# Kernel optimization log

Hardware: AMD Instinct MI355X
Metric: run time of the kernel (lower is better)

The kernel has to match this reference:

```python
import jax, jax.numpy as jnp
import numpy as np

K = 1  # Op(k=1): num = num_op // k == num_op, so random.sample selects ALL ops (deterministic)


def setup_inputs() -> dict:
    key = jax.random.key(0)
    k1, k2, k3, k4, k5 = jax.random.split(key, 5)
    N, D = 50000, 128
    NUM_OP, E = 8, 400000
    return {
        "x": jax.random.normal(k1, (N, D), dtype=jnp.float32),
        "edge_vals": jax.random.uniform(k2, (NUM_OP, E), dtype=jnp.float32),
        "ws": jax.random.uniform(k3, (NUM_OP,), dtype=jnp.float32),
        "edge_rows": jax.random.randint(k4, (NUM_OP, E), 0, N, dtype=jnp.int32),
        "edge_cols": jax.random.randint(k5, (NUM_OP, E), 0, N, dtype=jnp.int32),
    }


def reference(x, edge_vals, ws, edge_rows, edge_cols):
    # out = (1/num) * sum_i ws[i] * spmm(A_i, x), with num = num_op (k=1 -> all ops sampled)
    N = x.shape[0]
    num_op = ws.shape[0]
    num = num_op // K
    out = jnp.zeros_like(x)
    for i in range(num_op):  # small fixed set of ops (NAS mixture), not a data dim
        msg = edge_vals[i][:, None] * x[edge_cols[i]]  # [E, D] gather + scale
        out = out + ws[i] * jax.ops.segment_sum(msg, edge_rows[i], num_segments=N)
    return out / num
```

## Files before the change

### kernel.cpp

```cpp
#include <hip/hip_runtime.h>


#define D_DIM 128
#define RPB_SHIFT 5
#define RPB 32
#define CSEG 16
#define CSEG_SHIFT 12
#define NB (RPB * CSEG)
#define MAXB 2048
#define CHUNK 8192
#define SCAN_BLOCK 1024
#define CVT_BLOCKS 1024
#define CNT_BLOCKS 256

typedef unsigned long long ull;

static __device__ __forceinline__ unsigned short f2bf(float f) {
    unsigned int u = __float_as_uint(f);
    u += 0x7FFFu + ((u >> 16) & 1u);
    return (unsigned short)(u >> 16);
}

static __device__ __forceinline__ ull pack2f(float a, float b) {
    return (ull)__float_as_uint(a) | ((ull)__float_as_uint(b) << 32);
}

__global__ __launch_bounds__(256) void spmm_scatter_kernel(
    const float* __restrict__ x, const float* __restrict__ edge_vals,
    const float* __restrict__ ws, const int* __restrict__ edge_rows,
    const int* __restrict__ edge_cols, float* __restrict__ out,
    int E, float inv_num)
{
    const int  op   = blockIdx.y;
    const long base = (long)op * (long)E;
    const float wscale = ws[op] * inv_num;
    const int lane = threadIdx.x & 63;
    const int wave = blockIdx.x * (blockDim.x >> 6) + (threadIdx.x >> 6);
    const int nwaves = gridDim.x * (blockDim.x >> 6);
    for (int e = wave; e < E; e += nwaves) {
        const int row = edge_rows[base + e];
        const int col = edge_cols[base + e];
        const float v = edge_vals[base + e] * wscale;
        const float2 xv = *reinterpret_cast<const float2*>(x + (long)col * D_DIM + lane * 2);
        float* o = out + (long)row * D_DIM + lane * 2;
        atomicAdd(o, xv.x * v);
        atomicAdd(o + 1, xv.y * v);
    }
}

__global__ __launch_bounds__(256) void convert_count_kernel(
    const float4* __restrict__ x4, ull* __restrict__ xh, int n4,
    const int* __restrict__ rows, int* __restrict__ gcount, long n, int B)
{
    __shared__ int h[MAXB];
    if (blockIdx.x < CVT_BLOCKS) {
        const int stride = CVT_BLOCKS * 256;
        for (int i = blockIdx.x * 256 + threadIdx.x; i < n4; i += stride) {
            const float4 v = x4[i];
            const ull p =
                (ull)f2bf(v.x)
                | ((ull)f2bf(v.y) << 16)
                | ((ull)f2bf(v.z) << 32)
                | ((ull)f2bf(v.w) << 48);
            xh[i] = p;
        }
    } else {
        const int cb = blockIdx.x - CVT_BLOCKS;
        for (int i = threadIdx.x; i < B; i += 256) h[i] = 0;
        __syncthreads();
        const long n4r = n >> 2;
        for (long q = (long)cb * 256 + threadIdx.x; q < n4r;
             q += (long)CNT_BLOCKS * 256) {
            const int4 r = reinterpret_cast<const int4*>(rows)[q];
            atomicAdd(&h[r.x >> RPB_SHIFT], 1);
            atomicAdd(&h[r.y >> RPB_SHIFT], 1);
            atomicAdd(&h[r.z >> RPB_SHIFT], 1);
            atomicAdd(&h[r.w >> RPB_SHIFT], 1);
        }
        if (cb == 0 && (long)threadIdx.x < (n & 3))
            atomicAdd(&h[rows[(n4r << 2) + threadIdx.x] >> RPB_SHIFT], 1);
        __syncthreads();
        for (int i = threadIdx.x; i < B; i += 256)
            if (h[i]) atomicAdd(&gcount[i], h[i]);
    }
}

__global__ __launch_bounds__(SCAN_BLOCK) void scan_kernel(
    int* __restrict__ cursors, int* __restrict__ offsets, int N)
{
    __shared__ int sdata[SCAN_BLOCK];
    __shared__ int carry_s;
    if (threadIdx.x == 0) carry_s = 0;
    __syncthreads();
    for (int base = 0; base < N; base += SCAN_BLOCK) {
        const int i = base + (int)threadIdx.x;
        const int v = (i < N) ? cursors[i] : 0;
        sdata[threadIdx.x] = v;
        __syncthreads();
        for (int ofs = 1; ofs < SCAN_BLOCK; ofs <<= 1) {
            int t = (threadIdx.x >= (unsigned)ofs) ? sdata[threadIdx.x - ofs] : 0;
            __syncthreads();
            sdata[threadIdx.x] += t;
            __syncthreads();
        }
        const int incl  = sdata[threadIdx.x];
        const int carry = carry_s;
        if (i < N) {
            const int excl = carry + incl - v;
            offsets[i] = excl;
            cursors[i] = excl;
        }
        __syncthreads();
        if (threadIdx.x == SCAN_BLOCK - 1) carry_s = carry + incl;
        __syncthreads();
    }
    if (threadIdx.x == 0) offsets[N] = carry_s;
}

__global__ __launch_bounds__(1024, 8) void scatter_bucket_kernel(
    const int* __restrict__ edge_rows, const int* __restrict__ edge_cols,
    const float* __restrict__ edge_vals, const float* __restrict__ ws,
    int* __restrict__ gcursor, ull* __restrict__ records,
    int E, float inv_num, int B)
{
    __shared__ int hist[MAXB];
    const int  op   = blockIdx.y;
    const long base = (long)op * (long)E;
    const int  e0   = blockIdx.x * CHUNK;
    const int  e1   = min(e0 + CHUNK, E);
    const float wscale = ws[op] * inv_num;
    const int  tid  = (int)threadIdx.x;
    const int*   erow = edge_rows + base;
    const int*   ecol = edge_cols + base;
    const float* eval = edge_vals + base;

    for (int i = tid; i < B; i += 1024) hist[i] = 0;
    __syncthreads();

    const int gA = e0 + tid * 4;
    const int gB = gA + 4096;
    int4 rA = make_int4(0, 0, 0, 0), rB = make_int4(0, 0, 0, 0);
    int  mA = 0, mB = 0;

    { const int rem = e1 - gA;
      if (rem >= 4) { rA = *reinterpret_cast<const int4*>(erow + gA); mA = 4; }
      else if (rem > 0) { mA = rem; rA.x = erow[gA];
          if (rem > 1) rA.y = erow[gA + 1];
          if (rem > 2) rA.z = erow[gA + 2]; } }
    { const int rem = e1 - gB;
      if (rem >= 4) { rB = *reinterpret_cast<const int4*>(erow + gB); mB = 4; }
      else if (rem > 0) { mB = rem; rB.x = erow[gB];
          if (rem > 1) rB.y = erow[gB + 1];
          if (rem > 2) rB.z = erow[gB + 2]; } }

    if (mA > 0) atomicAdd(&hist[rA.x >> RPB_SHIFT], 1);
    if (mA > 1) atomicAdd(&hist[rA.y >> RPB_SHIFT], 1);
    if (mA > 2) atomicAdd(&hist[rA.z >> RPB_SHIFT], 1);
    if (mA > 3) atomicAdd(&hist[rA.w >> RPB_SHIFT], 1);
    if (mB > 0) atomicAdd(&hist[rB.x >> RPB_SHIFT], 1);
    if (mB > 1) atomicAdd(&hist[rB.y >> RPB_SHIFT], 1);
    if (mB > 2) atomicAdd(&hist[rB.z >> RPB_SHIFT], 1);
    if (mB > 3) atomicAdd(&hist[rB.w >> RPB_SHIFT], 1);
    __syncthreads();

    for (int i = tid; i < B; i += 1024) {
        const int c = hist[i];
        hist[i] = c ? atomicAdd(&gcursor[i], c) : 0;
    }
    __syncthreads();

#define EMIT(RW, CW, VW)                                                       \
    { const int bin_ = (RW) >> RPB_SHIFT;                                      \
      const int pos_ = atomicAdd(&hist[bin_], 1);                              \
      const ull rec_ = ((ull)__float_as_uint((VW) * wscale) << 32)             \
          | ((unsigned int)((RW) & (RPB - 1)) << 16) | (unsigned int)(CW);     \
      records[pos_] = rec_; }

    if (mA > 0) {
        int4 c = make_int4(0, 0, 0, 0); float4 v = make_float4(0.f, 0.f, 0.f, 0.f);
        if (mA == 4) { c = *reinterpret_cast<const int4*>(ecol + gA);
                       v = *reinterpret_cast<const float4*>(eval + gA); }
        else { c.x = ecol[gA]; v.x = eval[gA];
               if (mA > 1) { c.y = ecol[gA + 1]; v.y = eval[gA + 1]; }
               if (mA > 2) { c.z = ecol[gA + 2]; v.z = eval[gA + 2]; } }
        EMIT(rA.x, c.x, v.x)
        if (mA > 1) EMIT(rA.y, c.y, v.y)
        if (mA > 2) EMIT(rA.z, c.z, v.z)
        if (mA > 3) EMIT(rA.w, c.w, v.w)
    }
    if (mB > 0) {
        int4 c = make_int4(0, 0, 0, 0); float4 v = make_float4(0.f, 0.f, 0.f, 0.f);
        if (mB == 4) { c = *reinterpret_cast<const int4*>(ecol + gB);
                       v = *reinterpret_cast<const float4*>(eval + gB); }
        else { c.x = ecol[gB]; v.x = eval[gB];
               if (mB > 1) { c.y = ecol[gB + 1]; v.y = eval[gB + 1]; }
               if (mB > 2) { c.z = ecol[gB + 2]; v.z = eval[gB + 2]; } }
        EMIT(rB.x, c.x, v.x)
        if (mB > 1) EMIT(rB.y, c.y, v.y)
        if (mB > 2) EMIT(rB.z, c.z, v.z)
        if (mB > 3) EMIT(rB.w, c.w, v.w)
    }
#undef EMIT
}

__global__ __launch_bounds__(256) void sort_bucket_kernel(
    const ull* __restrict__ records, ull* __restrict__ sorted,
    const int* __restrict__ boff, int* __restrict__ rowoff, int N, int B)
{
    __shared__ int h[NB];
    __shared__ int cur[NB];
    __shared__ int sA[NB], sB[NB];
    const int bkt   = blockIdx.x;
    const int start = boff[bkt], end = boff[bkt + 1];
    const int row0  = bkt << RPB_SHIFT;
    const int tid   = (int)threadIdx.x;

    for (int i = tid; i < NB; i += 256) h[i] = 0;
    __syncthreads();
    for (int i = start + tid; i < end; i += 256) {
        const unsigned int lo = (unsigned int)records[i];
        const int bin = (int)((lo >> 16) << 4) | (int)((lo & 0xFFFFu) >> CSEG_SHIFT);
        atomicAdd(&h[bin], 1);
    }
    __syncthreads();
    for (int i = tid; i < NB; i += 256) sA[i] = h[i];
    __syncthreads();
    int* src = sA; int* dst = sB;
    for (int ofs = 1; ofs < NB; ofs <<= 1) {
        for (int i = tid; i < NB; i += 256)
            dst[i] = src[i] + ((i >= ofs) ? src[i - ofs] : 0);
        __syncthreads();
        int* t = src; src = dst; dst = t;
    }
    for (int i = tid; i < NB; i += 256) cur[i] = start + src[i] - h[i];
    if (tid < RPB) {
        const int row = row0 + tid;
        if (row <= N) rowoff[row] = start + src[tid * CSEG] - h[tid * CSEG];
    }
    if (tid == 0 && bkt == B - 1 && row0 + RPB <= N)
        rowoff[N] = end;
    __syncthreads();
    for (int i = start + tid; i < end; i += 256) {
        const ull r = records[i];
        const unsigned int lo = (unsigned int)r;
        const int bin = (int)((lo >> 16) << 4) | (int)((lo & 0xFFFFu) >> CSEG_SHIFT);
        const int pos = atomicAdd(&cur[bin], 1);
        sorted[pos] = r;
    }
}

#define GPROC(R)                                                               \
    {                                                                          \
        const unsigned int col_ = (unsigned int)(R)&0xFFFFu;                   \
        const float v_ = __uint_as_float((unsigned int)((R) >> 32));           \
        const unsigned int p_ = *reinterpret_cast<const unsigned int*>(        \
            xh + (size_t)col_ * D_DIM + lane * 2);                             \
        ax += v_ * __uint_as_float(p_ << 16);                                  \
        ay += v_ * __uint_as_float(p_ & 0xFFFF0000u);                          \
    }

__global__ __launch_bounds__(256) void gather_sorted_kernel(
    const unsigned short* __restrict__ xh, const int* __restrict__ rowoff,
    const ull* __restrict__ sorted, float* __restrict__ out, int N)
{
    const int lane = threadIdx.x & 63;
    const int row  = blockIdx.x * 4 + (threadIdx.x >> 6);
    if (row >= N) return;

    const int start = __builtin_amdgcn_readfirstlane(rowoff[row]);
    const int end   = __builtin_amdgcn_readfirstlane(rowoff[row + 1]);

    float ax = 0.f, ay = 0.f;
    int j = start;
    for (; j + 7 < end; j += 8) {
        const ull r0 = sorted[j];
        const ull r1 = sorted[j + 1];
        const ull r2 = sorted[j + 2];
        const ull r3 = sorted[j + 3];
        const ull r4 = sorted[j + 4];
        const ull r5 = sorted[j + 5];
        const ull r6 = sorted[j + 6];
        const ull r7 = sorted[j + 7];
        GPROC(r0) GPROC(r1) GPROC(r2) GPROC(r3)
        GPROC(r4) GPROC(r5) GPROC(r6) GPROC(r7)
    }
    for (; j < end; ++j) {
        const ull r0 = sorted[j];
        GPROC(r0)
    }
    __builtin_nontemporal_store(pack2f(ax, ay),
        reinterpret_cast<ull*>(out + (size_t)row * D_DIM + lane * 2));
}

__global__ __launch_bounds__(1024) void gather_filter2_kernel(
    const unsigned short* __restrict__ xh, const int* __restrict__ boff,
    const ull* __restrict__ records, float* __restrict__ out, int N)
{
    const int lane = threadIdx.x & 63;
    const int wv   = threadIdx.x >> 6;
    const int bkt  = blockIdx.x;
    const int row0 = (bkt << RPB_SHIFT) + wv * 2;
    const int row1 = row0 + 1;
    const int start = boff[bkt], end = boff[bkt + 1];

    float a0x = 0.f, a0y = 0.f, a1x = 0.f, a1y = 0.f;
    for (int c = start; c < end; c += 64) {
        const int idx = c + lane;
        unsigned int lo = 0xFFFF0000u, hi = 0;
        if (idx < end) {
            const ull r = __builtin_nontemporal_load(&records[idx]);
            lo = (unsigned int)r;
            hi = (unsigned int)(r >> 32);
        }
        ull mask = __ballot((lo >> 17) == (unsigned int)wv);
        while (mask) {
            const int j = __ffsll(mask) - 1;
            mask &= mask - 1;
            const unsigned int lj = __shfl(lo, j);
            const float v = __uint_as_float(__shfl(hi, j));
            const unsigned int col = lj & 0xFFFFu;
            const unsigned int p = *reinterpret_cast<const unsigned int*>(
                xh + (size_t)col * D_DIM + lane * 2);
            const float px = __uint_as_float(p << 16);
            const float py = __uint_as_float(p & 0xFFFF0000u);
            if (lj & 0x10000u) { a1x += v * px; a1y += v * py; }
            else               { a0x += v * px; a0y += v * py; }
        }
    }
    if (row0 < N)
        __builtin_nontemporal_store(pack2f(a0x, a0y),
            reinterpret_cast<ull*>(out + (size_t)row0 * D_DIM + lane * 2));
    if (row1 < N)
        __builtin_nontemporal_store(pack2f(a1x, a1y),
            reinterpret_cast<ull*>(out + (size_t)row1 * D_DIM + lane * 2));
}

extern "C" void kernel_launch(void* const* d_in, const int* in_sizes, int n_in,
                              void* d_out, int out_size, void* d_ws, size_t ws_size,
                              hipStream_t stream)
{
    const float* x         = (const float*)d_in[0];
    const float* edge_vals = (const float*)d_in[1];
    const float* ws        = (const float*)d_in[2];
    const int*   edge_rows = (const int*)d_in[3];
    const int*   edge_cols = (const int*)d_in[4];
    float*       out       = (float*)d_out;

    const int num_op = in_sizes[2];
    const int E      = in_sizes[1] / num_op;
    const int N      = in_sizes[0] / D_DIM;
    const long Etot  = (long)num_op * (long)E;
    const int  B     = (N + RPB - 1) / RPB;
    const float inv_num = 1.0f / (float)num_op;

    const size_t off_boff    = 0;
    const size_t off_gcur    = ((size_t)(B + 1) * 4 + 255) & ~(size_t)255;
    const size_t off_rowoff  = (off_gcur + (size_t)B * 4 + 255) & ~(size_t)255;
    const size_t off_xh      = (off_rowoff + (size_t)(N + 1) * 4 + 255) & ~(size_t)255;
    const size_t off_records = (off_xh + (size_t)N * D_DIM * 2 + 255) & ~(size_t)255;
    const size_t off_sorted  = off_records + (size_t)Etot * 8;
    const size_t need_sort   = off_sorted + (size_t)Etot * 8;
    const size_t need_filter = off_sorted;

    if (ws_size < need_filter || B > MAXB || N > 65535) {
        (void)hipMemsetAsync(d_out, 0, (size_t)out_size * sizeof(float), stream);
        dim3 grid(256, num_op, 1);
        spmm_scatter_kernel<<<grid, 256, 0, stream>>>(
            x, edge_vals, ws, edge_rows, edge_cols, out, E, inv_num);
        return;
    }

    int* boff    = (int*)((char*)d_ws + off_boff);
    int* gcursor = (int*)((char*)d_ws + off_gcur);
    int* rowoff  = (int*)((char*)d_ws + off_rowoff);
    unsigned short* xh = (unsigned short*)((char*)d_ws + off_xh);
    ull* records = (ull*)((char*)d_ws + off_records);
    ull* sorted  = (ull*)((char*)d_ws + off_sorted);

    (void)hipMemsetAsync(gcursor, 0, (size_t)B * 4, stream);

    convert_count_kernel<<<CVT_BLOCKS + CNT_BLOCKS, 256, 0, stream>>>(
        (const float4*)x, (ull*)xh, N * D_DIM / 4, edge_rows, gcursor, Etot, B);
    scan_kernel<<<1, SCAN_BLOCK, 0, stream>>>(gcursor, boff, B);

    dim3 sgrid((E + CHUNK - 1) / CHUNK, num_op, 1);
    scatter_bucket_kernel<<<sgrid, 1024, 0, stream>>>(
        edge_rows, edge_cols, edge_vals, ws, gcursor, records, E, inv_num, B);

    if (ws_size >= need_sort) {
        sort_bucket_kernel<<<B, 256, 0, stream>>>(records, sorted, boff, rowoff, N, B);
        gather_sorted_kernel<<<(N + 3) / 4, 256, 0, stream>>>(xh, rowoff, sorted, out, N);
    } else {
        gather_filter2_kernel<<<B, 1024, 0, stream>>>(xh, boff, records, out, N);
    }
}
```

Baseline: 185.4 us.

## Compact sorted records to 32 bits and gather per column segment across rows

The sort kernel now uses 512 threads with a wave-shuffle scan and emits 32-bit records that pack a 16-bit column with a bf16-rounded value, and it stores per-(row, column-segment) bin offsets. The new gather kernel has each wave accumulate 8 rows and walk column segments in lockstep, so the x rows it gathers at the same time come from nearby columns and can reuse cache. This halves sorted-record traffic and aims to improve L2 locality of the x gathers. The cost is that edge values are rounded to bf16, which adds some error, and each wave now does more per-bin offset loads and serial loop overhead.

```diff
diff --git a/kernel.cpp b/kernel.cpp
--- a/kernel.cpp
+++ b/kernel.cpp
@@ -203,93 +203,116 @@
 #undef EMIT
 }
 
-__global__ __launch_bounds__(256) void sort_bucket_kernel(
-    const ull* __restrict__ records, ull* __restrict__ sorted,
-    const int* __restrict__ boff, int* __restrict__ rowoff, int N, int B)
+__global__ __launch_bounds__(512) void sort_bucket_kernel(
+    const ull* __restrict__ records, unsigned int* __restrict__ sorted32,
+    const int* __restrict__ boff, int* __restrict__ binoff, int N, int B)
 {
     __shared__ int h[NB];
     __shared__ int cur[NB];
-    __shared__ int sA[NB], sB[NB];
+    __shared__ int wsum[8];
+    __shared__ int woff[8];
     const int bkt   = blockIdx.x;
     const int start = boff[bkt], end = boff[bkt + 1];
-    const int row0  = bkt << RPB_SHIFT;
     const int tid   = (int)threadIdx.x;
-
-    for (int i = tid; i < NB; i += 256) h[i] = 0;
-    __syncthreads();
-    for (int i = start + tid; i < end; i += 256) {
+    const int lane  = tid & 63;
+    const int w     = tid >> 6;
+
+    h[tid] = 0;
+    __syncthreads();
+    for (int i = start + tid; i < end; i += 512) {
         const unsigned int lo = (unsigned int)records[i];
         const int bin = (int)((lo >> 16) << 4) | (int)((lo & 0xFFFFu) >> CSEG_SHIFT);
         atomicAdd(&h[bin], 1);
     }
     __syncthreads();
-    for (int i = tid; i < NB; i += 256) sA[i] = h[i];
-    __syncthreads();
-    int* src = sA; int* dst = sB;
-    for (int ofs = 1; ofs < NB; ofs <<= 1) {
-        for (int i = tid; i < NB; i += 256)
-            dst[i] = src[i] + ((i >= ofs) ? src[i - ofs] : 0);
-        __syncthreads();
-        int* t = src; src = dst; dst = t;
-    }
-    for (int i = tid; i < NB; i += 256) cur[i] = start + src[i] - h[i];
-    if (tid < RPB) {
-        const int row = row0 + tid;
-        if (row <= N) rowoff[row] = start + src[tid * CSEG] - h[tid * CSEG];
-    }
-    if (tid == 0 && bkt == B - 1 && row0 + RPB <= N)
-        rowoff[N] = end;
-    __syncthreads();
-    for (int i = start + tid; i < end; i += 256) {
+    const int v = h[tid];
+    int incl = v;
+    #pragma unroll
+    for (int o = 1; o < 64; o <<= 1) {
+        const int t = __shfl_up(incl, o);
+        if (lane >= o) incl += t;
+    }
+    if (lane == 63) wsum[w] = incl;
+    __syncthreads();
+    if (tid == 0) {
+        int run = 0;
+        #pragma unroll
+        for (int k = 0; k < 8; ++k) { woff[k] = run; run += wsum[k]; }
+    }
+    __syncthreads();
+    const int excl = start + woff[w] + incl - v;
+    cur[tid] = excl;
+    binoff[bkt * NB + tid] = excl;
+    if (tid == 0 && bkt == B - 1) binoff[B * NB] = end;
+    __syncthreads();
+    for (int i = start + tid; i < end; i += 512) {
         const ull r = records[i];
         const unsigned int lo = (unsigned int)r;
         const int bin = (int)((lo >> 16) << 4) | (int)((lo & 0xFFFFu) >> CSEG_SHIFT);
         const int pos = atomicAdd(&cur[bin], 1);
-        sorted[pos] = r;
-    }
-}
-
-#define GPROC(R)                                                               \
-    {                                                                          \
-        const unsigned int col_ = (unsigned int)(R)&0xFFFFu;                   \
-        const float v_ = __uint_as_float((unsigned int)((R) >> 32));           \
-        const unsigned int p_ = *reinterpret_cast<const unsigned int*>(        \
-            xh + (size_t)col_ * D_DIM + lane * 2);                             \
-        ax += v_ * __uint_as_float(p_ << 16);                                  \
-        ay += v_ * __uint_as_float(p_ & 0xFFFF0000u);                          \
-    }
-
-__global__ __launch_bounds__(256) void gather_sorted_kernel(
-    const unsigned short* __restrict__ xh, const int* __restrict__ rowoff,
-    const ull* __restrict__ sorted, float* __restrict__ out, int N)
-{
-    const int lane = threadIdx.x & 63;
-    const int row  = blockIdx.x * 4 + (threadIdx.x >> 6);
-    if (row >= N) return;
-
-    const int start = __builtin_amdgcn_readfirstlane(rowoff[row]);
-    const int end   = __builtin_amdgcn_readfirstlane(rowoff[row + 1]);
-
-    float ax = 0.f, ay = 0.f;
-    int j = start;
-    for (; j + 7 < end; j += 8) {
-        const ull r0 = sorted[j];
-        const ull r1 = sorted[j + 1];
-        const ull r2 = sorted[j + 2];
-        const ull r3 = sorted[j + 3];
-        const ull r4 = sorted[j + 4];
-        const ull r5 = sorted[j + 5];
-        const ull r6 = sorted[j + 6];
-        const ull r7 = sorted[j + 7];
-        GPROC(r0) GPROC(r1) GPROC(r2) GPROC(r3)
-        GPROC(r4) GPROC(r5) GPROC(r6) GPROC(r7)
-    }
-    for (; j < end; ++j) {
-        const ull r0 = sorted[j];
-        GPROC(r0)
-    }
-    __builtin_nontemporal_store(pack2f(ax, ay),
-        reinterpret_cast<ull*>(out + (size_t)row * D_DIM + lane * 2));
+        sorted32[pos] = (lo & 0xFFFFu)
+            | ((unsigned int)f2bf(__uint_as_float((unsigned int)(r >> 32))) << 16);
+    }
+}
+
+__global__ __launch_bounds__(512) void gather_seg_kernel(
+    const unsigned short* __restrict__ xh, const int* __restrict__ binoff,
+    const unsigned int* __restrict__ sorted32, float* __restrict__ out,
+    int N, int B)
+{
+    const int tid  = (int)threadIdx.x;
+    const int lane = tid & 63;
+    const int w    = tid >> 6;
+    const int bkt  = blockIdx.x * 2 + (w >> 2);
+    if (bkt >= B) return;
+    const int rl0  = (w & 3) * 8;
+    const int bb   = bkt * NB + rl0 * CSEG;
+
+    float accx[8], accy[8];
+    #pragma unroll
+    for (int rr = 0; rr < 8; ++rr) { accx[rr] = 0.f; accy[rr] = 0.f; }
+
+    for (int seg = 0; seg < CSEG; ++seg) {
+        #pragma unroll
+        for (int rr = 0; rr < 8; ++rr) {
+            const int jb = __builtin_amdgcn_readfirstlane(
+                binoff[bb + rr * CSEG + seg]);
+            const int je = __builtin_amdgcn_readfirstlane(
+                binoff[bb + rr * CSEG + seg + 1]);
+            int j = jb;
+            for (; j + 1 < je; j += 2) {
+                const unsigned int r0 = sorted32[j];
+                const unsigned int r1 = sorted32[j + 1];
+                const unsigned int p0 = *reinterpret_cast<const unsigned int*>(
+                    xh + (size_t)(r0 & 0xFFFFu) * D_DIM + lane * 2);
+                const unsigned int p1 = *reinterpret_cast<const unsigned int*>(
+                    xh + (size_t)(r1 & 0xFFFFu) * D_DIM + lane * 2);
+                const float v0 = __uint_as_float(r0 & 0xFFFF0000u);
+                const float v1 = __uint_as_float(r1 & 0xFFFF0000u);
+                accx[rr] += v0 * __uint_as_float(p0 << 16)
+                          + v1 * __uint_as_float(p1 << 16);
+                accy[rr] += v0 * __uint_as_float(p0 & 0xFFFF0000u)
+                          + v1 * __uint_as_float(p1 & 0xFFFF0000u);
+            }
+            if (j < je) {
+                const unsigned int r0 = sorted32[j];
+                const unsigned int p0 = *reinterpret_cast<const unsigned int*>(
+                    xh + (size_t)(r0 & 0xFFFFu) * D_DIM + lane * 2);
+                const float v0 = __uint_as_float(r0 & 0xFFFF0000u);
+                accx[rr] += v0 * __uint_as_float(p0 << 16);
+                accy[rr] += v0 * __uint_as_float(p0 & 0xFFFF0000u);
+            }
+        }
+    }
+
+    const int row0 = (bkt << RPB_SHIFT) + rl0;
+    #pragma unroll
+    for (int rr = 0; rr < 8; ++rr) {
+        const int row = row0 + rr;
+        if (row < N)
+            __builtin_nontemporal_store(pack2f(accx[rr], accy[rr]),
+                reinterpret_cast<ull*>(out + (size_t)row * D_DIM + lane * 2));
+    }
 }
 
 __global__ __launch_bounds__(1024) void gather_filter2_kernel(
@@ -355,11 +378,11 @@
 
     const size_t off_boff    = 0;
     const size_t off_gcur    = ((size_t)(B + 1) * 4 + 255) & ~(size_t)255;
-    const size_t off_rowoff  = (off_gcur + (size_t)B * 4 + 255) & ~(size_t)255;
-    const size_t off_xh      = (off_rowoff + (size_t)(N + 1) * 4 + 255) & ~(size_t)255;
+    const size_t off_binoff  = (off_gcur + (size_t)B * 4 + 255) & ~(size_t)255;
+    const size_t off_xh      = (off_binoff + ((size_t)B * NB + 1) * 4 + 255) & ~(size_t)255;
     const size_t off_records = (off_xh + (size_t)N * D_DIM * 2 + 255) & ~(size_t)255;
     const size_t off_sorted  = off_records + (size_t)Etot * 8;
-    const size_t need_sort   = off_sorted + (size_t)Etot * 8;
+    const size_t need_sort   = off_sorted + (size_t)Etot * 4;
     const size_t need_filter = off_sorted;
 
     if (ws_size < need_filter || B > MAXB || N > 65535) {
@@ -372,10 +395,10 @@
 
     int* boff    = (int*)((char*)d_ws + off_boff);
     int* gcursor = (int*)((char*)d_ws + off_gcur);
-    int* rowoff  = (int*)((char*)d_ws + off_rowoff);
+    int* binoff  = (int*)((char*)d_ws + off_binoff);
     unsigned short* xh = (unsigned short*)((char*)d_ws + off_xh);
     ull* records = (ull*)((char*)d_ws + off_records);
-    ull* sorted  = (ull*)((char*)d_ws + off_sorted);
+    unsigned int* sorted32 = (unsigned int*)((char*)d_ws + off_sorted);
 
     (void)hipMemsetAsync(gcursor, 0, (size_t)B * 4, stream);
 
@@ -388,8 +411,10 @@
         edge_rows, edge_cols, edge_vals, ws, gcursor, records, E, inv_num, B);
 
     if (ws_size >= need_sort) {
-        sort_bucket_kernel<<<B, 256, 0, stream>>>(records, sorted, boff, rowoff, N, B);
-        gather_sorted_kernel<<<(N + 3) / 4, 256, 0, stream>>>(xh, rowoff, sorted, out, N);
+        sort_bucket_kernel<<<B, 512, 0, stream>>>(
+            records, sorted32, boff, binoff, N, B);
+        gather_seg_kernel<<<(B + 1) / 2, 512, 0, stream>>>(
+            xh, binoff, sorted32, out, N, B);
     } else {
         gather_filter2_kernel<<<B, 1024, 0, stream>>>(xh, boff, records, out, N);
     }
```

After: 244.0 us. 1.32x slower.
